# Kernel optimization log

Measured on AMD Instinct MI355X. Metric: run time of the kernel, lower is better.

Reference implementation:

```python
import jax, jax.numpy as jnp
import numpy as np

H = 512   # hidden_size
T = 256   # sequence_length
L = 2     # num_layers
IN = 5    # input_size (hardcoded in module)
NC = 2    # num_classes


def _lstm_layer(x, w_ih, w_hh, b):
    """One LSTM layer, batch_first. x: [B,T,D]; w_ih: [4H,D]; w_hh: [4H,H]; b: [4H].
    PyTorch gate order: i, f, g, o."""
    xp = jnp.einsum('btd,gd->btg', x, w_ih) + b  # [B,T,4H] input projections, hoisted out of scan
    B = x.shape[0]
    h0 = jnp.zeros((B, H), x.dtype)

    def step(carry, xt):
        h, c = carry
        gates = xt + h @ w_hh.T
        i, f, g, o = jnp.split(gates, 4, axis=-1)
        c = jax.nn.sigmoid(f) * c + jax.nn.sigmoid(i) * jnp.tanh(g)
        h = jax.nn.sigmoid(o) * jnp.tanh(c)
        return (h, c), h

    _, hs = jax.lax.scan(step, (h0, h0), jnp.swapaxes(xp, 0, 1))  # hs: [T,B,H]
    return jnp.swapaxes(hs, 0, 1)  # [B,T,H]


def setup_inputs() -> dict:
    key = jax.random.key(0)
    ks = jax.random.split(key, 16)
    s_in = 1.0 / np.sqrt(H)
    inp = {
        'x_time': jax.random.normal(ks[0], (256, T, IN), jnp.float32),
        'x_stat': jax.random.normal(ks[1], (256, 3), jnp.float32),
        # LSTM layer 0 (input_size=5) and layer 1 (input_size=H); biases b_ih+b_hh folded into one.
        'w_ih0': jax.random.uniform(ks[2], (4 * H, IN), jnp.float32, -s_in, s_in),
        'w_hh0': jax.random.uniform(ks[3], (4 * H, H), jnp.float32, -s_in, s_in),
        'b0': jax.random.uniform(ks[4], (4 * H,), jnp.float32, -s_in, s_in),
        'w_ih1': jax.random.uniform(ks[5], (4 * H, H), jnp.float32, -s_in, s_in),
        'w_hh1': jax.random.uniform(ks[6], (4 * H, H), jnp.float32, -s_in, s_in),
        'b1': jax.random.uniform(ks[7], (4 * H,), jnp.float32, -s_in, s_in),
        'fc1_w': jax.random.uniform(ks[8], (NC, H * T), jnp.float32, -0.01, 0.01),
        'fc1_b': jax.random.uniform(ks[9], (NC,), jnp.float32, -0.01, 0.01),
        'fc2_w': jax.random.uniform(ks[10], (NC, 3), jnp.float32, -0.5, 0.5),
        'fc2_b': jax.random.uniform(ks[11], (NC,), jnp.float32, -0.5, 0.5),
        'fc3_w': jax.random.uniform(ks[12], (NC, 4), jnp.float32, -0.5, 0.5),
        'fc3_b': jax.random.uniform(ks[13], (NC,), jnp.float32, -0.5, 0.5),
    }
    return inp


def reference(x_time, x_stat, w_ih0, w_hh0, b0, w_ih1, w_hh1, b1,
              fc1_w, fc1_b, fc2_w, fc2_b, fc3_w, fc3_b):
    B = x_time.shape[0]
    h = _lstm_layer(x_time, w_ih0, w_hh0, b0)     # [B,T,H]
    lstm_out = _lstm_layer(h, w_ih1, w_hh1, b1)   # [B,T,H]
    stat_preds = x_stat.reshape(B, -1) @ fc2_w.T + fc2_b          # [B,2]
    time_preds = lstm_out.reshape(B, -1) @ fc1_w.T + fc1_b        # [B,2]
    preds = jnp.concatenate([stat_preds, time_preds], axis=1)     # [B,4]
    preds = preds @ fc3_w.T + fc3_b                               # [B,2]
    return preds.reshape(B, -1)
```

## Files before the change

kernel.cpp:

```cpp
#include <hip/hip_runtime.h>
#include <hip/hip_bf16.h>
#include <math.h>

#define Bc 256
#define Tc 256
#define Hc 512
#define INc 5

typedef __bf16 bf16x8 __attribute__((ext_vector_type(8)));
typedef float f32x4 __attribute__((ext_vector_type(4)));

__device__ __forceinline__ float sigmoidf_(float x) {
    return 1.0f / (1.0f + __expf(-x));
}
__device__ __forceinline__ float tanhf_(float x) {
    float ax = fabsf(x);
    float e = __expf(2.0f * ax);
    float t = 1.0f - 2.0f / (e + 1.0f);
    return copysignf(t, x);
}

__device__ __forceinline__ void seg(f32x4 acc[2][2],
                                    const __hip_bfloat16* __restrict__ A,
                                    const __hip_bfloat16* __restrict__ W,
                                    int b0i, int wrow0, int lane)
{
    const int lrow = lane & 15;
    const int koff = (lane >> 4) * 8;
    const bf16x8* pa0 = reinterpret_cast<const bf16x8*>(A + (size_t)(b0i + lrow) * Hc + koff);
    const bf16x8* pa1 = reinterpret_cast<const bf16x8*>(A + (size_t)(b0i + 16 + lrow) * Hc + koff);
    const bf16x8* pb0 = reinterpret_cast<const bf16x8*>(W + (size_t)(wrow0 + lrow) * Hc + koff);
    const bf16x8* pb1 = reinterpret_cast<const bf16x8*>(W + (size_t)(wrow0 + 16 + lrow) * Hc + koff);
#pragma unroll
    for (int kk = 0; kk < 16; kk++) {
        bf16x8 a0 = pa0[kk * 4];
        bf16x8 a1 = pa1[kk * 4];
        bf16x8 w0 = pb0[kk * 4];
        bf16x8 w1 = pb1[kk * 4];
        acc[0][0] = __builtin_amdgcn_mfma_f32_16x16x32_bf16(a0, w0, acc[0][0], 0, 0, 0);
        acc[0][1] = __builtin_amdgcn_mfma_f32_16x16x32_bf16(a0, w1, acc[0][1], 0, 0, 0);
        acc[1][0] = __builtin_amdgcn_mfma_f32_16x16x32_bf16(a1, w0, acc[1][0], 0, 0, 0);
        acc[1][1] = __builtin_amdgcn_mfma_f32_16x16x32_bf16(a1, w1, acc[1][1], 0, 0, 0);
    }
}

__global__ __launch_bounds__(256) void lstm_step_mfma(
    const float* __restrict__ x_time, const float* __restrict__ w_ih0,
    const float* __restrict__ b0v, const float* __restrict__ b1v,
    const float* __restrict__ fc1_w,
    const __hip_bfloat16* __restrict__ wbf_hh0,
    const __hip_bfloat16* __restrict__ wbf_ih1,
    const __hip_bfloat16* __restrict__ wbf_hh1,
    const __hip_bfloat16* __restrict__ h0r, __hip_bfloat16* __restrict__ h0w,
    float* __restrict__ c0,
    const __hip_bfloat16* __restrict__ h1r, __hip_bfloat16* __restrict__ h1w,
    float* __restrict__ c1,
    float* __restrict__ partial,
    int t0, int t1, int l0, int l1)
{
    const int layer = blockIdx.x >> 7;
    const int bid = blockIdx.x & 127;
    if (layer == 0 && !l0) return;
    if (layer == 1 && !l1) return;

    const int bb = bid >> 4, jb = bid & 15;
    const int b0i = bb * 32, j0 = jb * 32;
    const int tid = threadIdx.x;
    const int lane = tid & 63;
    const int g = tid >> 6;

    __shared__ float gl[4][32][33];

    f32x4 acc[2][2] = {{{0.f, 0.f, 0.f, 0.f}, {0.f, 0.f, 0.f, 0.f}},
                       {{0.f, 0.f, 0.f, 0.f}, {0.f, 0.f, 0.f, 0.f}}};
    const int wrow0 = g * Hc + j0;

    if (layer == 0) {
        seg(acc, h0r, wbf_hh0, b0i, wrow0, lane);
    } else {
        seg(acc, h1r, wbf_hh1, b0i, wrow0, lane);
        seg(acc, h0r, wbf_ih1, b0i, wrow0, lane);
    }

    const int lrow = lane & 15, lgrp = lane >> 4;
#pragma unroll
    for (int bi = 0; bi < 2; bi++)
#pragma unroll
        for (int ji = 0; ji < 2; ji++)
#pragma unroll
            for (int r = 0; r < 4; r++)
                gl[g][16 * bi + lgrp * 4 + r][16 * ji + lrow] = acc[bi][ji][r];
    __syncthreads();

    const int bl = tid >> 3, j4 = tid & 7;
    const int b = b0i + bl;

    if (layer == 0) {
        float xv[INc];
#pragma unroll
        for (int d = 0; d < INc; d++)
            xv[d] = x_time[((size_t)b * Tc + t0) * INc + d];
#pragma unroll
        for (int jj = 0; jj < 4; jj++) {
            const int jl = j4 * 4 + jj, j = j0 + jl;
            float pre[4];
#pragma unroll
            for (int gg = 0; gg < 4; gg++) {
                const int row = gg * Hc + j;
                float s = gl[gg][bl][jl] + b0v[row];
#pragma unroll
                for (int d = 0; d < INc; d++)
                    s = fmaf(xv[d], w_ih0[(size_t)row * INc + d], s);
                pre[gg] = s;
            }
            float ig = sigmoidf_(pre[0]);
            float fg = sigmoidf_(pre[1]);
            float gv = tanhf_(pre[2]);
            float og = sigmoidf_(pre[3]);
            float c = fg * c0[(size_t)b * Hc + j] + ig * gv;
            c0[(size_t)b * Hc + j] = c;
            h0w[(size_t)b * Hc + j] = __float2bfloat16(og * tanhf_(c));
        }
    } else {
        float v0 = 0.f, v1 = 0.f;
#pragma unroll
        for (int jj = 0; jj < 4; jj++) {
            const int jl = j4 * 4 + jj, j = j0 + jl;
            float pre[4];
#pragma unroll
            for (int gg = 0; gg < 4; gg++)
                pre[gg] = gl[gg][bl][jl] + b1v[gg * Hc + j];
            float ig = sigmoidf_(pre[0]);
            float fg = sigmoidf_(pre[1]);
            float gv = tanhf_(pre[2]);
            float og = sigmoidf_(pre[3]);
            float c = fg * c1[(size_t)b * Hc + j] + ig * gv;
            c1[(size_t)b * Hc + j] = c;
            float h = og * tanhf_(c);
            h1w[(size_t)b * Hc + j] = __float2bfloat16(h);
            v0 = fmaf(h, fc1_w[(size_t)t1 * Hc + j], v0);
            v1 = fmaf(h, fc1_w[(size_t)Tc * Hc + (size_t)t1 * Hc + j], v1);
        }
#pragma unroll
        for (int off = 1; off < 8; off <<= 1) {
            v0 += __shfl_xor(v0, off);
            v1 += __shfl_xor(v1, off);
        }
        if (j4 == 0) {
            float* p = &partial[((size_t)jb * Bc + b) * 2];
            p[0] += v0;
            p[1] += v1;
        }
    }
}

__global__ void convert_weights(const float* __restrict__ w_hh0,
                                const float* __restrict__ w_ih1,
                                const float* __restrict__ w_hh1,
                                __hip_bfloat16* __restrict__ o0,
                                __hip_bfloat16* __restrict__ o1,
                                __hip_bfloat16* __restrict__ o2)
{
    const int i = blockIdx.x * blockDim.x + threadIdx.x;
    o0[i] = __float2bfloat16(w_hh0[i]);
    o1[i] = __float2bfloat16(w_ih1[i]);
    o2[i] = __float2bfloat16(w_hh1[i]);
}

__global__ void finalize_kernel(const float* __restrict__ x_stat,
                                const float* __restrict__ fc1_b,
                                const float* __restrict__ fc2_w, const float* __restrict__ fc2_b,
                                const float* __restrict__ fc3_w, const float* __restrict__ fc3_b,
                                const float* __restrict__ partial, float* __restrict__ out)
{
    const int b = threadIdx.x;
    float t0 = fc1_b[0], t1 = fc1_b[1];
    for (int jg = 0; jg < 16; jg++) {
        t0 += partial[((size_t)jg * Bc + b) * 2 + 0];
        t1 += partial[((size_t)jg * Bc + b) * 2 + 1];
    }
    const float s0 = fc2_b[0] + x_stat[b * 3 + 0] * fc2_w[0] + x_stat[b * 3 + 1] * fc2_w[1] + x_stat[b * 3 + 2] * fc2_w[2];
    const float s1 = fc2_b[1] + x_stat[b * 3 + 0] * fc2_w[3] + x_stat[b * 3 + 1] * fc2_w[4] + x_stat[b * 3 + 2] * fc2_w[5];
    out[b * 2 + 0] = fc3_b[0] + fc3_w[0] * s0 + fc3_w[1] * s1 + fc3_w[2] * t0 + fc3_w[3] * t1;
    out[b * 2 + 1] = fc3_b[1] + fc3_w[4] * s0 + fc3_w[5] * s1 + fc3_w[6] * t0 + fc3_w[7] * t1;
}

extern "C" void kernel_launch(void* const* d_in, const int* in_sizes, int n_in,
                              void* d_out, int out_size, void* d_ws, size_t ws_size,
                              hipStream_t stream)
{
    const float* x_time = (const float*)d_in[0];
    const float* x_stat = (const float*)d_in[1];
    const float* w_ih0 = (const float*)d_in[2];
    const float* w_hh0 = (const float*)d_in[3];
    const float* b0    = (const float*)d_in[4];
    const float* w_ih1 = (const float*)d_in[5];
    const float* w_hh1 = (const float*)d_in[6];
    const float* b1    = (const float*)d_in[7];
    const float* fc1_w = (const float*)d_in[8];
    const float* fc1_b = (const float*)d_in[9];
    const float* fc2_w = (const float*)d_in[10];
    const float* fc2_b = (const float*)d_in[11];
    const float* fc3_w = (const float*)d_in[12];
    const float* fc3_b = (const float*)d_in[13];

    char* base = (char*)d_ws;
    const size_t WSZ = (size_t)4 * Hc * Hc;
    __hip_bfloat16* wbf_hh0 = (__hip_bfloat16*)base;
    __hip_bfloat16* wbf_ih1 = wbf_hh0 + WSZ;
    __hip_bfloat16* wbf_hh1 = wbf_ih1 + WSZ;
    __hip_bfloat16* h0 = wbf_hh1 + WSZ;
    __hip_bfloat16* h1 = h0 + (size_t)2 * Bc * Hc;
    float* c0 = (float*)(h1 + (size_t)2 * Bc * Hc);
    float* c1 = c0 + (size_t)Bc * Hc;
    float* partial = c1 + (size_t)Bc * Hc;

    const size_t zoff = (size_t)3 * WSZ * sizeof(__hip_bfloat16);
    const size_t zlen = (size_t)4 * Bc * Hc * sizeof(__hip_bfloat16)
                      + (size_t)2 * Bc * Hc * sizeof(float)
                      + (size_t)16 * Bc * 2 * sizeof(float);
    hipMemsetAsync(base + zoff, 0, zlen, stream);

    convert_weights<<<4096, 256, 0, stream>>>(w_hh0, w_ih1, w_hh1, wbf_hh0, wbf_ih1, wbf_hh1);

    for (int i = 0; i <= Tc; i++) {
        const int p = i & 1;
        const __hip_bfloat16* h0r = h0 + (size_t)p * Bc * Hc;
        __hip_bfloat16* h0wp      = h0 + (size_t)(p ^ 1) * Bc * Hc;
        const __hip_bfloat16* h1r = h1 + (size_t)(p ^ 1) * Bc * Hc;
        __hip_bfloat16* h1wp      = h1 + (size_t)p * Bc * Hc;
        lstm_step_mfma<<<256, 256, 0, stream>>>(
            x_time, w_ih0, b0, b1, fc1_w,
            wbf_hh0, wbf_ih1, wbf_hh1,
            h0r, h0wp, c0, h1r, h1wp, c1, partial,
            i, i - 1, (i < Tc) ? 1 : 0, (i >= 1) ? 1 : 0);
    }
    finalize_kernel<<<1, 256, 0, stream>>>(x_stat, fc1_b, fc2_w, fc2_b, fc3_w, fc3_b,
                                           partial, (float*)d_out);
}
```

Measured before the change: 5.026 ms.

## Replace per-timestep launches with persistent kernel using grid barriers and register-resident weights

```diff
diff --git a/kernel.cpp b/kernel.cpp
--- a/kernel.cpp
+++ b/kernel.cpp
@@ -6,6 +6,8 @@
 #define Tc 256
 #define Hc 512
 #define INc 5
+#define BH (Bc * Hc)
+#define NB 256
 
 typedef __bf16 bf16x8 __attribute__((ext_vector_type(8)));
 typedef float f32x4 __attribute__((ext_vector_type(4)));
@@ -19,127 +21,227 @@
     float t = 1.0f - 2.0f / (e + 1.0f);
     return copysignf(t, x);
 }
-
-__device__ __forceinline__ void seg(f32x4 acc[2][2],
-                                    const __hip_bfloat16* __restrict__ A,
-                                    const __hip_bfloat16* __restrict__ W,
-                                    int b0i, int wrow0, int lane)
-{
-    const int lrow = lane & 15;
-    const int koff = (lane >> 4) * 8;
-    const bf16x8* pa0 = reinterpret_cast<const bf16x8*>(A + (size_t)(b0i + lrow) * Hc + koff);
-    const bf16x8* pa1 = reinterpret_cast<const bf16x8*>(A + (size_t)(b0i + 16 + lrow) * Hc + koff);
-    const bf16x8* pb0 = reinterpret_cast<const bf16x8*>(W + (size_t)(wrow0 + lrow) * Hc + koff);
-    const bf16x8* pb1 = reinterpret_cast<const bf16x8*>(W + (size_t)(wrow0 + 16 + lrow) * Hc + koff);
-#pragma unroll
-    for (int kk = 0; kk < 16; kk++) {
-        bf16x8 a0 = pa0[kk * 4];
-        bf16x8 a1 = pa1[kk * 4];
-        bf16x8 w0 = pb0[kk * 4];
-        bf16x8 w1 = pb1[kk * 4];
-        acc[0][0] = __builtin_amdgcn_mfma_f32_16x16x32_bf16(a0, w0, acc[0][0], 0, 0, 0);
-        acc[0][1] = __builtin_amdgcn_mfma_f32_16x16x32_bf16(a0, w1, acc[0][1], 0, 0, 0);
-        acc[1][0] = __builtin_amdgcn_mfma_f32_16x16x32_bf16(a1, w0, acc[1][0], 0, 0, 0);
-        acc[1][1] = __builtin_amdgcn_mfma_f32_16x16x32_bf16(a1, w1, acc[1][1], 0, 0, 0);
+__device__ __forceinline__ unsigned short bfbits(float x) {
+    unsigned int u = __builtin_bit_cast(unsigned int, x);
+    unsigned int r = u + 0x7FFFu + ((u >> 16) & 1u);
+    return (unsigned short)(r >> 16);
+}
+
+__device__ __forceinline__ void gbar(int* cnt, int gen, int tid) {
+    __threadfence();
+    __syncthreads();
+    if (tid == 0) {
+        __hip_atomic_fetch_add(cnt, 1, __ATOMIC_RELEASE, __HIP_MEMORY_SCOPE_AGENT);
+        const int target = NB * gen;
+        while (__hip_atomic_load(cnt, __ATOMIC_ACQUIRE, __HIP_MEMORY_SCOPE_AGENT) < target)
+            __builtin_amdgcn_s_sleep(1);
     }
-}
-
-__global__ __launch_bounds__(256) void lstm_step_mfma(
+    __syncthreads();
+}
+
+__global__ void __launch_bounds__(256, 1) lstm_persist(
     const float* __restrict__ x_time, const float* __restrict__ w_ih0,
     const float* __restrict__ b0v, const float* __restrict__ b1v,
-    const float* __restrict__ fc1_w,
+    const float* __restrict__ fc1_w, const float* __restrict__ fc1_b,
+    const float* __restrict__ x_stat,
+    const float* __restrict__ fc2_w, const float* __restrict__ fc2_b,
+    const float* __restrict__ fc3_w, const float* __restrict__ fc3_b,
     const __hip_bfloat16* __restrict__ wbf_hh0,
-    const __hip_bfloat16* __restrict__ wbf_ih1,
-    const __hip_bfloat16* __restrict__ wbf_hh1,
-    const __hip_bfloat16* __restrict__ h0r, __hip_bfloat16* __restrict__ h0w,
-    float* __restrict__ c0,
-    const __hip_bfloat16* __restrict__ h1r, __hip_bfloat16* __restrict__ h1w,
-    float* __restrict__ c1,
-    float* __restrict__ partial,
-    int t0, int t1, int l0, int l1)
+    const __hip_bfloat16* __restrict__ wcat1,
+    __hip_bfloat16* h0, __hip_bfloat16* h1,
+    float* __restrict__ partial, int* bar, float* __restrict__ out)
 {
     const int layer = blockIdx.x >> 7;
     const int bid = blockIdx.x & 127;
-    if (layer == 0 && !l0) return;
-    if (layer == 1 && !l1) return;
-
     const int bb = bid >> 4, jb = bid & 15;
     const int b0i = bb * 32, j0 = jb * 32;
-    const int tid = threadIdx.x;
-    const int lane = tid & 63;
-    const int g = tid >> 6;
+    const int tid = threadIdx.x, lane = tid & 63, g = tid >> 6;
+    const int lrow = lane & 15, lgrp = lane >> 4;
+    const int koff = lgrp * 8;
 
     __shared__ float gl[4][32][33];
-
-    f32x4 acc[2][2] = {{{0.f, 0.f, 0.f, 0.f}, {0.f, 0.f, 0.f, 0.f}},
-                       {{0.f, 0.f, 0.f, 0.f}, {0.f, 0.f, 0.f, 0.f}}};
-    const int wrow0 = g * Hc + j0;
-
-    if (layer == 0) {
-        seg(acc, h0r, wbf_hh0, b0i, wrow0, lane);
-    } else {
-        seg(acc, h1r, wbf_hh1, b0i, wrow0, lane);
-        seg(acc, h0r, wbf_ih1, b0i, wrow0, lane);
+    __shared__ float wih_s[4][32][INc];
+    __shared__ float bias_s[4][32];
+
+    {
+        const float* bsrc = (layer == 0) ? b0v : b1v;
+        for (int idx = tid; idx < 128; idx += 256) {
+            int gg = idx >> 5, jl = idx & 31;
+            bias_s[gg][jl] = bsrc[gg * Hc + j0 + jl];
+        }
+        if (layer == 0) {
+            for (int idx = tid; idx < 4 * 32 * INc; idx += 256) {
+                int gg = idx / (32 * INc), r = idx % (32 * INc);
+                int jl = r / INc, d = r % INc;
+                wih_s[gg][jl][d] = w_ih0[(size_t)(gg * Hc + j0 + jl) * INc + d];
+            }
+        }
     }
-
-    const int lrow = lane & 15, lgrp = lane >> 4;
-#pragma unroll
-    for (int bi = 0; bi < 2; bi++)
-#pragma unroll
-        for (int ji = 0; ji < 2; ji++)
-#pragma unroll
-            for (int r = 0; r < 4; r++)
-                gl[g][16 * bi + lgrp * 4 + r][16 * ji + lrow] = acc[bi][ji][r];
     __syncthreads();
 
     const int bl = tid >> 3, j4 = tid & 7;
     const int b = b0i + bl;
+    float c_r[4] = {0.f, 0.f, 0.f, 0.f};
 
     if (layer == 0) {
-        float xv[INc];
-#pragma unroll
-        for (int d = 0; d < INc; d++)
-            xv[d] = x_time[((size_t)b * Tc + t0) * INc + d];
-#pragma unroll
-        for (int jj = 0; jj < 4; jj++) {
-            const int jl = j4 * 4 + jj, j = j0 + jl;
-            float pre[4];
-#pragma unroll
-            for (int gg = 0; gg < 4; gg++) {
-                const int row = gg * Hc + j;
-                float s = gl[gg][bl][jl] + b0v[row];
+        bf16x8 wr0[16], wr1[16];
+        {
+            const bf16x8* p0 = reinterpret_cast<const bf16x8*>(
+                wbf_hh0 + (size_t)(g * Hc + j0 + lrow) * Hc + koff);
+            const bf16x8* p1 = reinterpret_cast<const bf16x8*>(
+                wbf_hh0 + (size_t)(g * Hc + j0 + 16 + lrow) * Hc + koff);
+#pragma unroll
+            for (int kk = 0; kk < 16; kk++) { wr0[kk] = p0[kk * 4]; wr1[kk] = p1[kk * 4]; }
+        }
+        for (int i = 0; i <= Tc; i++) {
+            if (i < Tc) {
+                const __hip_bfloat16* h0r = h0 + (size_t)(i & 1) * BH;
+                __hip_bfloat16* h0w = h0 + (size_t)((i & 1) ^ 1) * BH;
+                float xv[INc];
 #pragma unroll
                 for (int d = 0; d < INc; d++)
-                    s = fmaf(xv[d], w_ih0[(size_t)row * INc + d], s);
-                pre[gg] = s;
+                    xv[d] = x_time[((size_t)b * Tc + i) * INc + d];
+
+                f32x4 a00 = {0,0,0,0}, a01 = {0,0,0,0}, a10 = {0,0,0,0}, a11 = {0,0,0,0};
+                const bf16x8* pa0 = reinterpret_cast<const bf16x8*>(
+                    h0r + (size_t)(b0i + lrow) * Hc + koff);
+                const bf16x8* pa1 = reinterpret_cast<const bf16x8*>(
+                    h0r + (size_t)(b0i + 16 + lrow) * Hc + koff);
+#pragma unroll
+                for (int kk = 0; kk < 16; kk++) {
+                    bf16x8 A0 = pa0[kk * 4], A1 = pa1[kk * 4];
+                    a00 = __builtin_amdgcn_mfma_f32_16x16x32_bf16(A0, wr0[kk], a00, 0, 0, 0);
+                    a01 = __builtin_amdgcn_mfma_f32_16x16x32_bf16(A0, wr1[kk], a01, 0, 0, 0);
+                    a10 = __builtin_amdgcn_mfma_f32_16x16x32_bf16(A1, wr0[kk], a10, 0, 0, 0);
+                    a11 = __builtin_amdgcn_mfma_f32_16x16x32_bf16(A1, wr1[kk], a11, 0, 0, 0);
+                }
+#pragma unroll
+                for (int r = 0; r < 4; r++) {
+                    gl[g][lgrp * 4 + r][lrow]          = a00[r];
+                    gl[g][lgrp * 4 + r][16 + lrow]     = a01[r];
+                    gl[g][16 + lgrp * 4 + r][lrow]     = a10[r];
+                    gl[g][16 + lgrp * 4 + r][16 + lrow] = a11[r];
+                }
+                __syncthreads();
+
+                unsigned int pk0 = 0, pk1 = 0;
+#pragma unroll
+                for (int jj = 0; jj < 4; jj++) {
+                    const int jl = j4 * 4 + jj;
+                    float pre[4];
+#pragma unroll
+                    for (int gg = 0; gg < 4; gg++) {
+                        float s = gl[gg][bl][jl] + bias_s[gg][jl];
+#pragma unroll
+                        for (int d = 0; d < INc; d++) s = fmaf(xv[d], wih_s[gg][jl][d], s);
+                        pre[gg] = s;
+                    }
+                    float ig = sigmoidf_(pre[0]), fg = sigmoidf_(pre[1]);
+                    float gv = tanhf_(pre[2]), og = sigmoidf_(pre[3]);
+                    float c = fg * c_r[jj] + ig * gv;
+                    c_r[jj] = c;
+                    float h = og * tanhf_(c);
+                    unsigned int hb = bfbits(h);
+                    if (jj == 0) pk0 = hb;
+                    else if (jj == 1) pk0 |= hb << 16;
+                    else if (jj == 2) pk1 = hb;
+                    else pk1 |= hb << 16;
+                }
+                *reinterpret_cast<uint2*>(h0w + (size_t)b * Hc + j0 + j4 * 4) =
+                    make_uint2(pk0, pk1);
             }
-            float ig = sigmoidf_(pre[0]);
-            float fg = sigmoidf_(pre[1]);
-            float gv = tanhf_(pre[2]);
-            float og = sigmoidf_(pre[3]);
-            float c = fg * c0[(size_t)b * Hc + j] + ig * gv;
-            c0[(size_t)b * Hc + j] = c;
-            h0w[(size_t)b * Hc + j] = __float2bfloat16(og * tanhf_(c));
+            gbar(bar, i + 1, tid);
+        }
+        gbar(bar, Tc + 2, tid);
+        if (blockIdx.x == 0) {
+            float t0s = fc1_b[0], t1s = fc1_b[1];
+            for (int jg = 0; jg < 16; jg++) {
+                t0s += partial[((size_t)jg * Bc + tid) * 2 + 0];
+                t1s += partial[((size_t)jg * Bc + tid) * 2 + 1];
+            }
+            float s0 = fc2_b[0] + x_stat[tid * 3 + 0] * fc2_w[0] + x_stat[tid * 3 + 1] * fc2_w[1] + x_stat[tid * 3 + 2] * fc2_w[2];
+            float s1 = fc2_b[1] + x_stat[tid * 3 + 0] * fc2_w[3] + x_stat[tid * 3 + 1] * fc2_w[4] + x_stat[tid * 3 + 2] * fc2_w[5];
+            out[tid * 2 + 0] = fc3_b[0] + fc3_w[0] * s0 + fc3_w[1] * s1 + fc3_w[2] * t0s + fc3_w[3] * t1s;
+            out[tid * 2 + 1] = fc3_b[1] + fc3_w[4] * s0 + fc3_w[5] * s1 + fc3_w[6] * t0s + fc3_w[7] * t1s;
         }
     } else {
+        bf16x8 wr0[32], wr1[32];
+        {
+            const bf16x8* p0 = reinterpret_cast<const bf16x8*>(
+                wcat1 + (size_t)(g * Hc + j0 + lrow) * 1024 + koff);
+            const bf16x8* p1 = reinterpret_cast<const bf16x8*>(
+                wcat1 + (size_t)(g * Hc + j0 + 16 + lrow) * 1024 + koff);
+#pragma unroll
+            for (int kk = 0; kk < 32; kk++) { wr0[kk] = p0[kk * 4]; wr1[kk] = p1[kk * 4]; }
+        }
         float v0 = 0.f, v1 = 0.f;
-#pragma unroll
-        for (int jj = 0; jj < 4; jj++) {
-            const int jl = j4 * 4 + jj, j = j0 + jl;
-            float pre[4];
-#pragma unroll
-            for (int gg = 0; gg < 4; gg++)
-                pre[gg] = gl[gg][bl][jl] + b1v[gg * Hc + j];
-            float ig = sigmoidf_(pre[0]);
-            float fg = sigmoidf_(pre[1]);
-            float gv = tanhf_(pre[2]);
-            float og = sigmoidf_(pre[3]);
-            float c = fg * c1[(size_t)b * Hc + j] + ig * gv;
-            c1[(size_t)b * Hc + j] = c;
-            float h = og * tanhf_(c);
-            h1w[(size_t)b * Hc + j] = __float2bfloat16(h);
-            v0 = fmaf(h, fc1_w[(size_t)t1 * Hc + j], v0);
-            v1 = fmaf(h, fc1_w[(size_t)Tc * Hc + (size_t)t1 * Hc + j], v1);
+        for (int i = 0; i <= Tc; i++) {
+            if (i >= 1) {
+                const int t1 = i - 1;
+                const __hip_bfloat16* h1r = h1 + (size_t)((i & 1) ^ 1) * BH;
+                __hip_bfloat16* h1w = h1 + (size_t)(i & 1) * BH;
+                const __hip_bfloat16* h0r = h0 + (size_t)(i & 1) * BH;
+                float wf0[4], wf1[4];
+                {
+                    const float* fp = fc1_w + (size_t)t1 * Hc + j0 + j4 * 4;
+#pragma unroll
+                    for (int jj = 0; jj < 4; jj++) {
+                        wf0[jj] = fp[jj];
+                        wf1[jj] = fp[(size_t)Tc * Hc + jj];
+                    }
+                }
+                f32x4 a00 = {0,0,0,0}, a01 = {0,0,0,0}, a10 = {0,0,0,0}, a11 = {0,0,0,0};
+                const bf16x8* pa0 = reinterpret_cast<const bf16x8*>(
+                    h1r + (size_t)(b0i + lrow) * Hc + koff);
+                const bf16x8* pa1 = reinterpret_cast<const bf16x8*>(
+                    h1r + (size_t)(b0i + 16 + lrow) * Hc + koff);
+                const bf16x8* pc0 = reinterpret_cast<const bf16x8*>(
+                    h0r + (size_t)(b0i + lrow) * Hc + koff);
+                const bf16x8* pc1 = reinterpret_cast<const bf16x8*>(
+                    h0r + (size_t)(b0i + 16 + lrow) * Hc + koff);
+#pragma unroll
+                for (int kk = 0; kk < 32; kk++) {
+                    bf16x8 A0 = (kk < 16) ? pa0[kk * 4] : pc0[(kk - 16) * 4];
+                    bf16x8 A1 = (kk < 16) ? pa1[kk * 4] : pc1[(kk - 16) * 4];
+                    a00 = __builtin_amdgcn_mfma_f32_16x16x32_bf16(A0, wr0[kk], a00, 0, 0, 0);
+                    a01 = __builtin_amdgcn_mfma_f32_16x16x32_bf16(A0, wr1[kk], a01, 0, 0, 0);
+                    a10 = __builtin_amdgcn_mfma_f32_16x16x32_bf16(A1, wr0[kk], a10, 0, 0, 0);
+                    a11 = __builtin_amdgcn_mfma_f32_16x16x32_bf16(A1, wr1[kk], a11, 0, 0, 0);
+                }
+#pragma unroll
+                for (int r = 0; r < 4; r++) {
+                    gl[g][lgrp * 4 + r][lrow]          = a00[r];
+                    gl[g][lgrp * 4 + r][16 + lrow]     = a01[r];
+                    gl[g][16 + lgrp * 4 + r][lrow]     = a10[r];
+                    gl[g][16 + lgrp * 4 + r][16 + lrow] = a11[r];
+                }
+                __syncthreads();
+
+                unsigned int pk0 = 0, pk1 = 0;
+#pragma unroll
+                for (int jj = 0; jj < 4; jj++) {
+                    const int jl = j4 * 4 + jj;
+                    float pre[4];
+#pragma unroll
+                    for (int gg = 0; gg < 4; gg++)
+                        pre[gg] = gl[gg][bl][jl] + bias_s[gg][jl];
+                    float ig = sigmoidf_(pre[0]), fg = sigmoidf_(pre[1]);
+                    float gv = tanhf_(pre[2]), og = sigmoidf_(pre[3]);
+                    float c = fg * c_r[jj] + ig * gv;
+                    c_r[jj] = c;
+                    float h = og * tanhf_(c);
+                    v0 = fmaf(h, wf0[jj], v0);
+                    v1 = fmaf(h, wf1[jj], v1);
+                    unsigned int hb = bfbits(h);
+                    if (jj == 0) pk0 = hb;
+                    else if (jj == 1) pk0 |= hb << 16;
+                    else if (jj == 2) pk1 = hb;
+                    else pk1 |= hb << 16;
+                }
+                *reinterpret_cast<uint2*>(h1w + (size_t)b * Hc + j0 + j4 * 4) =
+                    make_uint2(pk0, pk1);
+            }
+            gbar(bar, i + 1, tid);
         }
 #pragma unroll
         for (int off = 1; off < 8; off <<= 1) {
@@ -147,42 +249,24 @@
             v1 += __shfl_xor(v1, off);
         }
         if (j4 == 0) {
-            float* p = &partial[((size_t)jb * Bc + b) * 2];
-            p[0] += v0;
-            p[1] += v1;
-        }
+            partial[((size_t)jb * Bc + b) * 2 + 0] = v0;
+            partial[((size_t)jb * Bc + b) * 2 + 1] = v1;
+        }
+        gbar(bar, Tc + 2, tid);
     }
 }
 
 __global__ void convert_weights(const float* __restrict__ w_hh0,
+                                const float* __restrict__ w_hh1,
                                 const float* __restrict__ w_ih1,
-                                const float* __restrict__ w_hh1,
-                                __hip_bfloat16* __restrict__ o0,
-                                __hip_bfloat16* __restrict__ o1,
-                                __hip_bfloat16* __restrict__ o2)
+                                __hip_bfloat16* __restrict__ o_hh0,
+                                __hip_bfloat16* __restrict__ o_cat)
 {
-    const int i = blockIdx.x * blockDim.x + threadIdx.x;
-    o0[i] = __float2bfloat16(w_hh0[i]);
-    o1[i] = __float2bfloat16(w_ih1[i]);
-    o2[i] = __float2bfloat16(w_hh1[i]);
-}
-
-__global__ void finalize_kernel(const float* __restrict__ x_stat,
-                                const float* __restrict__ fc1_b,
-                                const float* __restrict__ fc2_w, const float* __restrict__ fc2_b,
-                                const float* __restrict__ fc3_w, const float* __restrict__ fc3_b,
-                                const float* __restrict__ partial, float* __restrict__ out)
-{
-    const int b = threadIdx.x;
-    float t0 = fc1_b[0], t1 = fc1_b[1];
-    for (int jg = 0; jg < 16; jg++) {
-        t0 += partial[((size_t)jg * Bc + b) * 2 + 0];
-        t1 += partial[((size_t)jg * Bc + b) * 2 + 1];
-    }
-    const float s0 = fc2_b[0] + x_stat[b * 3 + 0] * fc2_w[0] + x_stat[b * 3 + 1] * fc2_w[1] + x_stat[b * 3 + 2] * fc2_w[2];
-    const float s1 = fc2_b[1] + x_stat[b * 3 + 0] * fc2_w[3] + x_stat[b * 3 + 1] * fc2_w[4] + x_stat[b * 3 + 2] * fc2_w[5];
-    out[b * 2 + 0] = fc3_b[0] + fc3_w[0] * s0 + fc3_w[1] * s1 + fc3_w[2] * t0 + fc3_w[3] * t1;
-    out[b * 2 + 1] = fc3_b[1] + fc3_w[4] * s0 + fc3_w[5] * s1 + fc3_w[6] * t0 + fc3_w[7] * t1;
+    const int i = blockIdx.x * 256 + threadIdx.x;
+    o_hh0[i] = __float2bfloat16(w_hh0[i]);
+    const int r = i >> 9, k = i & 511;
+    o_cat[(size_t)r * 1024 + k] = __float2bfloat16(w_hh1[i]);
+    o_cat[(size_t)r * 1024 + 512 + k] = __float2bfloat16(w_ih1[i]);
 }
 
 extern "C" void kernel_launch(void* const* d_in, const int* in_sizes, int n_in,
@@ -204,37 +288,22 @@
     const float* fc3_w = (const float*)d_in[12];
     const float* fc3_b = (const float*)d_in[13];
 
-    char* base = (char*)d_ws;
-    const size_t WSZ = (size_t)4 * Hc * Hc;
-    __hip_bfloat16* wbf_hh0 = (__hip_bfloat16*)base;
-    __hip_bfloat16* wbf_ih1 = wbf_hh0 + WSZ;
-    __hip_bfloat16* wbf_hh1 = wbf_ih1 + WSZ;
-    __hip_bfloat16* h0 = wbf_hh1 + WSZ;
-    __hip_bfloat16* h1 = h0 + (size_t)2 * Bc * Hc;
-    float* c0 = (float*)(h1 + (size_t)2 * Bc * Hc);
-    float* c1 = c0 + (size_t)Bc * Hc;
-    float* partial = c1 + (size_t)Bc * Hc;
-
-    const size_t zoff = (size_t)3 * WSZ * sizeof(__hip_bfloat16);
-    const size_t zlen = (size_t)4 * Bc * Hc * sizeof(__hip_bfloat16)
-                      + (size_t)2 * Bc * Hc * sizeof(float)
-                      + (size_t)16 * Bc * 2 * sizeof(float);
-    hipMemsetAsync(base + zoff, 0, zlen, stream);
-
-    convert_weights<<<4096, 256, 0, stream>>>(w_hh0, w_ih1, w_hh1, wbf_hh0, wbf_ih1, wbf_hh1);
-
-    for (int i = 0; i <= Tc; i++) {
-        const int p = i & 1;
-        const __hip_bfloat16* h0r = h0 + (size_t)p * Bc * Hc;
-        __hip_bfloat16* h0wp      = h0 + (size_t)(p ^ 1) * Bc * Hc;
-        const __hip_bfloat16* h1r = h1 + (size_t)(p ^ 1) * Bc * Hc;
-        __hip_bfloat16* h1wp      = h1 + (size_t)p * Bc * Hc;
-        lstm_step_mfma<<<256, 256, 0, stream>>>(
-            x_time, w_ih0, b0, b1, fc1_w,
-            wbf_hh0, wbf_ih1, wbf_hh1,
-            h0r, h0wp, c0, h1r, h1wp, c1, partial,
-            i, i - 1, (i < Tc) ? 1 : 0, (i >= 1) ? 1 : 0);
-    }
-    finalize_kernel<<<1, 256, 0, stream>>>(x_stat, fc1_b, fc2_w, fc2_b, fc3_w, fc3_b,
-                                           partial, (float*)d_out);
-}
+    __hip_bfloat16* wbf_hh0 = (__hip_bfloat16*)d_ws;
+    __hip_bfloat16* wcat1 = wbf_hh0 + (size_t)2048 * 512;
+    __hip_bfloat16* h0p = wcat1 + (size_t)2048 * 1024;
+    __hip_bfloat16* h1p = h0p + (size_t)2 * BH;
+    float* partialp = (float*)(h1p + (size_t)2 * BH);
+    int* barp = (int*)(partialp + (size_t)16 * Bc * 2);
+
+    const size_t zoff = ((size_t)2048 * 512 + (size_t)2048 * 1024) * sizeof(__hip_bfloat16);
+    const size_t zlen = (size_t)4 * BH * sizeof(__hip_bfloat16)
+                      + (size_t)16 * Bc * 2 * sizeof(float) + 256;
+    hipMemsetAsync((char*)d_ws + zoff, 0, zlen, stream);
+
+    convert_weights<<<4096, 256, 0, stream>>>(w_hh0, w_hh1, w_ih1, wbf_hh0, wcat1);
+
+    lstm_persist<<<NB, 256, 0, stream>>>(
+        x_time, w_ih0, b0, b1, fc1_w, fc1_b, x_stat,
+        fc2_w, fc2_b, fc3_w, fc3_b,
+        wbf_hh0, wcat1, h0p, h1p, partialp, barp, (float*)d_out);
+}
```

Result: slower. 13.43 ms (+167.3%).

## Split LSTM step into smaller tiles with more blocks and concatenated layer-1 weights

Applied to the files above, without the earlier changes.

```diff
diff --git a/kernel.cpp b/kernel.cpp
--- a/kernel.cpp
+++ b/kernel.cpp
@@ -6,6 +6,8 @@
 #define Tc 256
 #define Hc 512
 #define INc 5
+#define BH (Bc * Hc)
+#define MFMA __builtin_amdgcn_mfma_f32_16x16x32_bf16
 
 typedef __bf16 bf16x8 __attribute__((ext_vector_type(8)));
 typedef float f32x4 __attribute__((ext_vector_type(4)));
@@ -19,38 +21,18 @@
     float t = 1.0f - 2.0f / (e + 1.0f);
     return copysignf(t, x);
 }
-
-__device__ __forceinline__ void seg(f32x4 acc[2][2],
-                                    const __hip_bfloat16* __restrict__ A,
-                                    const __hip_bfloat16* __restrict__ W,
-                                    int b0i, int wrow0, int lane)
-{
-    const int lrow = lane & 15;
-    const int koff = (lane >> 4) * 8;
-    const bf16x8* pa0 = reinterpret_cast<const bf16x8*>(A + (size_t)(b0i + lrow) * Hc + koff);
-    const bf16x8* pa1 = reinterpret_cast<const bf16x8*>(A + (size_t)(b0i + 16 + lrow) * Hc + koff);
-    const bf16x8* pb0 = reinterpret_cast<const bf16x8*>(W + (size_t)(wrow0 + lrow) * Hc + koff);
-    const bf16x8* pb1 = reinterpret_cast<const bf16x8*>(W + (size_t)(wrow0 + 16 + lrow) * Hc + koff);
-#pragma unroll
-    for (int kk = 0; kk < 16; kk++) {
-        bf16x8 a0 = pa0[kk * 4];
-        bf16x8 a1 = pa1[kk * 4];
-        bf16x8 w0 = pb0[kk * 4];
-        bf16x8 w1 = pb1[kk * 4];
-        acc[0][0] = __builtin_amdgcn_mfma_f32_16x16x32_bf16(a0, w0, acc[0][0], 0, 0, 0);
-        acc[0][1] = __builtin_amdgcn_mfma_f32_16x16x32_bf16(a0, w1, acc[0][1], 0, 0, 0);
-        acc[1][0] = __builtin_amdgcn_mfma_f32_16x16x32_bf16(a1, w0, acc[1][0], 0, 0, 0);
-        acc[1][1] = __builtin_amdgcn_mfma_f32_16x16x32_bf16(a1, w1, acc[1][1], 0, 0, 0);
-    }
-}
-
-__global__ __launch_bounds__(256) void lstm_step_mfma(
-    const float* __restrict__ x_time, const float* __restrict__ w_ih0,
-    const float* __restrict__ b0v, const float* __restrict__ b1v,
-    const float* __restrict__ fc1_w,
+__device__ __forceinline__ unsigned short bfbits(float x) {
+    unsigned int u = __builtin_bit_cast(unsigned int, x);
+    unsigned int r = u + 0x7FFFu + ((u >> 16) & 1u);
+    return (unsigned short)(r >> 16);
+}
+
+__global__ __launch_bounds__(512, 4) void lstm_step(
+    const float* __restrict__ x_time, const float* __restrict__ b0v,
+    const float* __restrict__ b1v, const float* __restrict__ fc1_w,
+    const float* __restrict__ w_ih0,
     const __hip_bfloat16* __restrict__ wbf_hh0,
-    const __hip_bfloat16* __restrict__ wbf_ih1,
-    const __hip_bfloat16* __restrict__ wbf_hh1,
+    const __hip_bfloat16* __restrict__ wcat1,
     const __hip_bfloat16* __restrict__ h0r, __hip_bfloat16* __restrict__ h0w,
     float* __restrict__ c0,
     const __hip_bfloat16* __restrict__ h1r, __hip_bfloat16* __restrict__ h1w,
@@ -58,95 +40,100 @@
     float* __restrict__ partial,
     int t0, int t1, int l0, int l1)
 {
-    const int layer = blockIdx.x >> 7;
-    const int bid = blockIdx.x & 127;
+    const int layer = blockIdx.x >> 8;
     if (layer == 0 && !l0) return;
     if (layer == 1 && !l1) return;
-
-    const int bb = bid >> 4, jb = bid & 15;
-    const int b0i = bb * 32, j0 = jb * 32;
-    const int tid = threadIdx.x;
-    const int lane = tid & 63;
-    const int g = tid >> 6;
-
-    __shared__ float gl[4][32][33];
-
-    f32x4 acc[2][2] = {{{0.f, 0.f, 0.f, 0.f}, {0.f, 0.f, 0.f, 0.f}},
-                       {{0.f, 0.f, 0.f, 0.f}, {0.f, 0.f, 0.f, 0.f}}};
-    const int wrow0 = g * Hc + j0;
-
+    const int bid = blockIdx.x & 255;
+    const int bb = bid >> 5, jb = bid & 31;
+    const int b0i = bb * 32, j0 = jb * 16;
+    const int tid = threadIdx.x, lane = tid & 63;
+    const int wid = tid >> 6, g = wid & 3, mh = wid >> 2;
+    const int lrow = lane & 15, lgrp = lane >> 4;
+
+    __shared__ float gl[4][32][17];
+    __shared__ float bias_s[64];
+    __shared__ float wih_s[320];
+
+    if (tid < 64)
+        bias_s[tid] = ((layer == 0) ? b0v : b1v)[(tid >> 4) * Hc + j0 + (tid & 15)];
+    if (layer == 0 && tid < 320) {
+        int gg = tid / 80, r = tid % 80, jl = r / INc, d = r % INc;
+        wih_s[(gg * 16 + jl) * INc + d] = w_ih0[(size_t)(gg * Hc + j0 + jl) * INc + d];
+    }
+
+    const int arow = b0i + mh * 16 + lrow;
+    f32x4 acc = {0.f, 0.f, 0.f, 0.f};
     if (layer == 0) {
-        seg(acc, h0r, wbf_hh0, b0i, wrow0, lane);
+        const __hip_bfloat16* pa = h0r + (size_t)arow * Hc + lgrp * 8;
+        const __hip_bfloat16* pb = wbf_hh0 + (size_t)(g * Hc + j0 + lrow) * Hc + lgrp * 8;
+#pragma unroll
+        for (int kc = 0; kc < 16; kc++) {
+            bf16x8 A = *reinterpret_cast<const bf16x8*>(pa + kc * 32);
+            bf16x8 B = *reinterpret_cast<const bf16x8*>(pb + kc * 32);
+            acc = MFMA(A, B, acc, 0, 0, 0);
+        }
     } else {
-        seg(acc, h1r, wbf_hh1, b0i, wrow0, lane);
-        seg(acc, h0r, wbf_ih1, b0i, wrow0, lane);
-    }
-
-    const int lrow = lane & 15, lgrp = lane >> 4;
-#pragma unroll
-    for (int bi = 0; bi < 2; bi++)
-#pragma unroll
-        for (int ji = 0; ji < 2; ji++)
-#pragma unroll
-            for (int r = 0; r < 4; r++)
-                gl[g][16 * bi + lgrp * 4 + r][16 * ji + lrow] = acc[bi][ji][r];
+        const __hip_bfloat16* pa1 = h1r + (size_t)arow * Hc + lgrp * 8;
+        const __hip_bfloat16* pa0 = h0r + (size_t)arow * Hc + lgrp * 8;
+        const __hip_bfloat16* pb = wcat1 + (size_t)(g * Hc + j0 + lrow) * 1024 + lgrp * 8;
+#pragma unroll
+        for (int kc = 0; kc < 16; kc++) {
+            bf16x8 A = *reinterpret_cast<const bf16x8*>(pa1 + kc * 32);
+            bf16x8 B = *reinterpret_cast<const bf16x8*>(pb + kc * 32);
+            acc = MFMA(A, B, acc, 0, 0, 0);
+        }
+#pragma unroll
+        for (int kc = 0; kc < 16; kc++) {
+            bf16x8 A = *reinterpret_cast<const bf16x8*>(pa0 + kc * 32);
+            bf16x8 B = *reinterpret_cast<const bf16x8*>(pb + 512 + kc * 32);
+            acc = MFMA(A, B, acc, 0, 0, 0);
+        }
+    }
+#pragma unroll
+    for (int r = 0; r < 4; r++)
+        gl[g][mh * 16 + lgrp * 4 + r][lrow] = acc[r];
     __syncthreads();
 
-    const int bl = tid >> 3, j4 = tid & 7;
-    const int b = b0i + bl;
+    const int bl = tid >> 4, jl = tid & 15;
+    const int b = b0i + bl, j = j0 + jl;
 
     if (layer == 0) {
-        float xv[INc];
-#pragma unroll
-        for (int d = 0; d < INc; d++)
-            xv[d] = x_time[((size_t)b * Tc + t0) * INc + d];
-#pragma unroll
-        for (int jj = 0; jj < 4; jj++) {
-            const int jl = j4 * 4 + jj, j = j0 + jl;
-            float pre[4];
-#pragma unroll
-            for (int gg = 0; gg < 4; gg++) {
-                const int row = gg * Hc + j;
-                float s = gl[gg][bl][jl] + b0v[row];
-#pragma unroll
-                for (int d = 0; d < INc; d++)
-                    s = fmaf(xv[d], w_ih0[(size_t)row * INc + d], s);
-                pre[gg] = s;
-            }
-            float ig = sigmoidf_(pre[0]);
-            float fg = sigmoidf_(pre[1]);
-            float gv = tanhf_(pre[2]);
-            float og = sigmoidf_(pre[3]);
-            float c = fg * c0[(size_t)b * Hc + j] + ig * gv;
-            c0[(size_t)b * Hc + j] = c;
-            h0w[(size_t)b * Hc + j] = __float2bfloat16(og * tanhf_(c));
-        }
+        float pre[4];
+#pragma unroll
+        for (int gg = 0; gg < 4; gg++)
+            pre[gg] = gl[gg][bl][jl] + bias_s[gg * 16 + jl];
+        const float* xp = x_time + ((size_t)b * Tc + t0) * INc;
+#pragma unroll
+        for (int d = 0; d < INc; d++) {
+            float xv = xp[d];
+#pragma unroll
+            for (int gg = 0; gg < 4; gg++)
+                pre[gg] = fmaf(xv, wih_s[(gg * 16 + jl) * INc + d], pre[gg]);
+        }
+        float ig = sigmoidf_(pre[0]), fg = sigmoidf_(pre[1]);
+        float gv = tanhf_(pre[2]), og = sigmoidf_(pre[3]);
+        float c = fg * c0[(size_t)b * Hc + j] + ig * gv;
+        c0[(size_t)b * Hc + j] = c;
+        h0w[(size_t)b * Hc + j] = __hip_bfloat16_raw{bfbits(og * tanhf_(c))};
     } else {
-        float v0 = 0.f, v1 = 0.f;
-#pragma unroll
-        for (int jj = 0; jj < 4; jj++) {
-            const int jl = j4 * 4 + jj, j = j0 + jl;
-            float pre[4];
-#pragma unroll
-            for (int gg = 0; gg < 4; gg++)
-                pre[gg] = gl[gg][bl][jl] + b1v[gg * Hc + j];
-            float ig = sigmoidf_(pre[0]);
-            float fg = sigmoidf_(pre[1]);
-            float gv = tanhf_(pre[2]);
-            float og = sigmoidf_(pre[3]);
-            float c = fg * c1[(size_t)b * Hc + j] + ig * gv;
-            c1[(size_t)b * Hc + j] = c;
-            float h = og * tanhf_(c);
-            h1w[(size_t)b * Hc + j] = __float2bfloat16(h);
-            v0 = fmaf(h, fc1_w[(size_t)t1 * Hc + j], v0);
-            v1 = fmaf(h, fc1_w[(size_t)Tc * Hc + (size_t)t1 * Hc + j], v1);
-        }
-#pragma unroll
-        for (int off = 1; off < 8; off <<= 1) {
+        float pre[4];
+#pragma unroll
+        for (int gg = 0; gg < 4; gg++)
+            pre[gg] = gl[gg][bl][jl] + bias_s[gg * 16 + jl];
+        float ig = sigmoidf_(pre[0]), fg = sigmoidf_(pre[1]);
+        float gv = tanhf_(pre[2]), og = sigmoidf_(pre[3]);
+        float c = fg * c1[(size_t)b * Hc + j] + ig * gv;
+        c1[(size_t)b * Hc + j] = c;
+        float h = og * tanhf_(c);
+        h1w[(size_t)b * Hc + j] = __hip_bfloat16_raw{bfbits(h)};
+        float v0 = h * fc1_w[(size_t)t1 * Hc + j];
+        float v1 = h * fc1_w[(size_t)Tc * Hc + (size_t)t1 * Hc + j];
+#pragma unroll
+        for (int off = 1; off < 16; off <<= 1) {
             v0 += __shfl_xor(v0, off);
             v1 += __shfl_xor(v1, off);
         }
-        if (j4 == 0) {
+        if (jl == 0) {
             float* p = &partial[((size_t)jb * Bc + b) * 2];
             p[0] += v0;
             p[1] += v1;
@@ -155,16 +142,16 @@
 }
 
 __global__ void convert_weights(const float* __restrict__ w_hh0,
+                                const float* __restrict__ w_hh1,
                                 const float* __restrict__ w_ih1,
-                                const float* __restrict__ w_hh1,
-                                __hip_bfloat16* __restrict__ o0,
-                                __hip_bfloat16* __restrict__ o1,
-                                __hip_bfloat16* __restrict__ o2)
-{
-    const int i = blockIdx.x * blockDim.x + threadIdx.x;
-    o0[i] = __float2bfloat16(w_hh0[i]);
-    o1[i] = __float2bfloat16(w_ih1[i]);
-    o2[i] = __float2bfloat16(w_hh1[i]);
+                                __hip_bfloat16* __restrict__ o_hh0,
+                                __hip_bfloat16* __restrict__ o_cat)
+{
+    const int i = blockIdx.x * 256 + threadIdx.x;
+    o_hh0[i] = __float2bfloat16(w_hh0[i]);
+    const int r = i >> 9, k = i & 511;
+    o_cat[(size_t)r * 1024 + k] = __float2bfloat16(w_hh1[i]);
+    o_cat[(size_t)r * 1024 + 512 + k] = __float2bfloat16(w_ih1[i]);
 }
 
 __global__ void finalize_kernel(const float* __restrict__ x_stat,
@@ -175,7 +162,7 @@
 {
     const int b = threadIdx.x;
     float t0 = fc1_b[0], t1 = fc1_b[1];
-    for (int jg = 0; jg < 16; jg++) {
+    for (int jg = 0; jg < 32; jg++) {
         t0 += partial[((size_t)jg * Bc + b) * 2 + 0];
         t1 += partial[((size_t)jg * Bc + b) * 2 + 1];
     }
@@ -204,37 +191,33 @@
     const float* fc3_w = (const float*)d_in[12];
     const float* fc3_b = (const float*)d_in[13];
 
-    char* base = (char*)d_ws;
-    const size_t WSZ = (size_t)4 * Hc * Hc;
-    __hip_bfloat16* wbf_hh0 = (__hip_bfloat16*)base;
-    __hip_bfloat16* wbf_ih1 = wbf_hh0 + WSZ;
-    __hip_bfloat16* wbf_hh1 = wbf_ih1 + WSZ;
-    __hip_bfloat16* h0 = wbf_hh1 + WSZ;
-    __hip_bfloat16* h1 = h0 + (size_t)2 * Bc * Hc;
-    float* c0 = (float*)(h1 + (size_t)2 * Bc * Hc);
-    float* c1 = c0 + (size_t)Bc * Hc;
-    float* partial = c1 + (size_t)Bc * Hc;
-
-    const size_t zoff = (size_t)3 * WSZ * sizeof(__hip_bfloat16);
-    const size_t zlen = (size_t)4 * Bc * Hc * sizeof(__hip_bfloat16)
-                      + (size_t)2 * Bc * Hc * sizeof(float)
-                      + (size_t)16 * Bc * 2 * sizeof(float);
-    hipMemsetAsync(base + zoff, 0, zlen, stream);
-
-    convert_weights<<<4096, 256, 0, stream>>>(w_hh0, w_ih1, w_hh1, wbf_hh0, wbf_ih1, wbf_hh1);
+    __hip_bfloat16* wbf_hh0 = (__hip_bfloat16*)d_ws;
+    __hip_bfloat16* wcat1 = wbf_hh0 + (size_t)2048 * 512;
+    __hip_bfloat16* h0p = wcat1 + (size_t)2048 * 1024;
+    __hip_bfloat16* h1p = h0p + (size_t)2 * BH;
+    float* c0p = (float*)(h1p + (size_t)2 * BH);
+    float* c1p = c0p + (size_t)BH;
+    float* partialp = c1p + (size_t)BH;
+
+    const size_t zoff = ((size_t)2048 * 512 + (size_t)2048 * 1024) * sizeof(__hip_bfloat16);
+    const size_t zlen = (size_t)4 * BH * sizeof(__hip_bfloat16)
+                      + (size_t)2 * BH * sizeof(float)
+                      + (size_t)32 * Bc * 2 * sizeof(float);
+    hipMemsetAsync((char*)d_ws + zoff, 0, zlen, stream);
+
+    convert_weights<<<4096, 256, 0, stream>>>(w_hh0, w_hh1, w_ih1, wbf_hh0, wcat1);
 
     for (int i = 0; i <= Tc; i++) {
         const int p = i & 1;
-        const __hip_bfloat16* h0r = h0 + (size_t)p * Bc * Hc;
-        __hip_bfloat16* h0wp      = h0 + (size_t)(p ^ 1) * Bc * Hc;
-        const __hip_bfloat16* h1r = h1 + (size_t)(p ^ 1) * Bc * Hc;
-        __hip_bfloat16* h1wp      = h1 + (size_t)p * Bc * Hc;
-        lstm_step_mfma<<<256, 256, 0, stream>>>(
-            x_time, w_ih0, b0, b1, fc1_w,
-            wbf_hh0, wbf_ih1, wbf_hh1,
-            h0r, h0wp, c0, h1r, h1wp, c1, partial,
+        const __hip_bfloat16* h0r = h0p + (size_t)p * BH;
+        __hip_bfloat16* h0wp      = h0p + (size_t)(p ^ 1) * BH;
+        const __hip_bfloat16* h1r = h1p + (size_t)(p ^ 1) * BH;
+        __hip_bfloat16* h1wp      = h1p + (size_t)p * BH;
+        lstm_step<<<512, 512, 0, stream>>>(
+            x_time, b0, b1, fc1_w, w_ih0, wbf_hh0, wcat1,
+            h0r, h0wp, c0p, h1r, h1wp, c1p, partialp,
             i, i - 1, (i < Tc) ? 1 : 0, (i >= 1) ? 1 : 0);
     }
     finalize_kernel<<<1, 256, 0, stream>>>(x_stat, fc1_b, fc2_w, fc2_b, fc3_w, fc3_b,
-                                           partial, (float*)d_out);
-}
+                                           partialp, (float*)d_out);
+}
```

Measured after the change: 6.430 ms. 27.9% more time.
